# Kernel optimization log

Hardware: AMD Instinct MI355X
Metric: run time of the kernel (lower is better)

Reference implementation:

```python
import jax, jax.numpy as jnp
import numpy as np

H, DK, DV = 16, 64, 64

def setup_inputs() -> dict:
    key = jax.random.key(0)
    ks = jax.random.split(key, 5)
    S, E = 2048, 1024
    return {
        "x": jax.random.normal(ks[0], (S, E), jnp.float32),
        "Wq": jax.random.normal(ks[1], (H * DK, E), jnp.float32) * 0.02,
        "Wk": jax.random.normal(ks[2], (H * DK, E), jnp.float32) * 0.02,
        "Wv": jax.random.normal(ks[3], (H * DV, E), jnp.float32) * 0.02,
        "Wo": jax.random.normal(ks[4], (H * DV, H * DV), jnp.float32) * 0.02,
    }

def reference(x, Wq, Wk, Wv, Wo):
    S = x.shape[0]
    # Fused QKV projections (equivalent to per-head Linear with concatenated weights)
    Q = (x @ Wq.T).reshape(S, H, DK).transpose(1, 0, 2)  # [H,S,dk]
    K = (x @ Wk.T).reshape(S, H, DK).transpose(1, 0, 2)  # [H,S,dk]
    V = (x @ Wv.T).reshape(S, H, DV).transpose(1, 0, 2)  # [H,S,dv]
    scale = 1.0 / np.sqrt(DK).astype(np.float32)
    scores = jnp.einsum('hsd,htd->hst', Q, K) * scale    # [H,S,S]
    weights = jax.nn.softmax(scores, axis=-1)
    A = jnp.einsum('hst,htv->hsv', weights, V)           # [H,S,dv]
    A1 = A.transpose(1, 0, 2).reshape(S, H * DV)         # concat heads on last dim
    return A1 @ Wo.T
```

## Files before the change

### kernel.cpp

```cpp
#include <hip/hip_runtime.h>
#include <hip/hip_bf16.h>
#include <stdint.h>

typedef uint16_t u16;
typedef uint32_t u32;
typedef float    f32x4  __attribute__((ext_vector_type(4)));
typedef __bf16   bf16x8 __attribute__((ext_vector_type(8)));
typedef uint16_t u16x8  __attribute__((ext_vector_type(8)));
typedef uint16_t u16x4  __attribute__((ext_vector_type(4)));
typedef uint32_t u32x4  __attribute__((ext_vector_type(4)));

#define HH 16
#define SS 2048
#define EE 1024
#define DD 64

__device__ inline u16 f2bf(float f) {
  uint32_t u = __builtin_bit_cast(uint32_t, f);
  u += 0x7fff + ((u >> 16) & 1);
  return (u16)(u >> 16);
}
__device__ inline float bf2f(u16 b) {
  return __builtin_bit_cast(float, (uint32_t)b << 16);
}

__device__ inline u32 cvtpk(float lo, float hi) {
  u32 r;
  asm("v_cvt_pk_bf16_f32 %0, %1, %2" : "=v"(r) : "v"(lo), "v"(hi));
  return r;
}

__device__ inline void gload_lds16(const void* g, void* l) {
  __builtin_amdgcn_global_load_lds(
      (const __attribute__((address_space(1))) uint32_t*)g,
      (__attribute__((address_space(3))) uint32_t*)l, 16, 0, 0);
}

__global__ __launch_bounds__(256) void convert_kernel(
    const float* __restrict__ x,  const float* __restrict__ wq,
    const float* __restrict__ wk, const float* __restrict__ wv,
    const float* __restrict__ wo,
    u16* __restrict__ xb, u16* __restrict__ wqkvb, u16* __restrict__ wob) {
  const int64_t M1 = 1024 * 1024;
  int64_t e = ((int64_t)blockIdx.x * 256 + threadIdx.x) * 4;
  const float* src; u16* dst; int64_t off;
  if (e < 2 * M1)      { src = x;  dst = xb;           off = e; }
  else if (e < 3 * M1) { src = wq; dst = wqkvb;        off = e - 2 * M1; }
  else if (e < 4 * M1) { src = wk; dst = wqkvb + M1;   off = e - 3 * M1; }
  else if (e < 5 * M1) { src = wv; dst = wqkvb + 2*M1; off = e - 4 * M1; }
  else                 { src = wo; dst = wob;          off = e - 5 * M1; }
  float4 v = *(const float4*)(src + off);
  u16x4 o;
  o[0] = f2bf(v.x); o[1] = f2bf(v.y); o[2] = f2bf(v.z); o[3] = f2bf(v.w);
  *(u16x4*)(dst + off) = o;
}

template <int EPI, int K, int N, int BN>
__global__ __launch_bounds__(256, 4) void gemm_kernel(
    const u16* __restrict__ A, const u16* __restrict__ B,
    u16* __restrict__ q_ws, u16* __restrict__ k_ws, u16* __restrict__ vt_ws,
    float* __restrict__ Cout) {
  constexpr int BM = 64, BK = 64;
  constexpr int NFB = BN / 32;
  constexpr float C2 = 0.18033688f;
  __shared__ __align__(16) u16 As[BM * BK];
  __shared__ __align__(16) u16 Bs[BN * BK];
  const int t = threadIdx.x;
  const int lane = t & 63, w = t >> 6;
  const int wr = w >> 1, wc = w & 1;
  const int fr = lane & 15, fg = lane >> 4;

  const int nwg = gridDim.x * gridDim.y;
  const int bid = blockIdx.y * gridDim.x + blockIdx.x;
  const int swz = (bid & 7) * (nwg >> 3) + (bid >> 3);
  const int m0 = (swz / gridDim.x) * BM, n0 = (swz % gridDim.x) * BN;

  f32x4 acc[2][NFB] = {};

  for (int k0 = 0; k0 < K; k0 += BK) {
#pragma unroll
    for (int it = 0; it < 2; ++it) {
      const int c = t + it * 256, row = c >> 3, sch = (c & 7) ^ (row & 7);
      gload_lds16(A + (int64_t)(m0 + row) * K + k0 + sch * 8,
                  As + (c & ~63) * 8);
    }
#pragma unroll
    for (int it = 0; it < BN * 8 / 256; ++it) {
      const int c = t + it * 256, row = c >> 3, sch = (c & 7) ^ (row & 7);
      gload_lds16(B + (int64_t)(n0 + row) * K + k0 + sch * 8,
                  Bs + (c & ~63) * 8);
    }
    __syncthreads();
    bf16x8 af[2][2], bfr[NFB][2];
#pragma unroll
    for (int mi = 0; mi < 2; ++mi)
#pragma unroll
      for (int kc = 0; kc < 2; ++kc) {
        const int row = wr * 32 + mi * 16 + fr;
        const int cc = (kc * 4 + fg) ^ (row & 7);
        af[mi][kc] = __builtin_bit_cast(bf16x8, *(const u16x8*)&As[row * 64 + cc * 8]);
      }
#pragma unroll
    for (int ni = 0; ni < NFB; ++ni)
#pragma unroll
      for (int kc = 0; kc < 2; ++kc) {
        const int row = wc * (BN / 2) + ni * 16 + fr;
        const int cc = (kc * 4 + fg) ^ (row & 7);
        bfr[ni][kc] = __builtin_bit_cast(bf16x8, *(const u16x8*)&Bs[row * 64 + cc * 8]);
      }
#pragma unroll
    for (int kc = 0; kc < 2; ++kc)
#pragma unroll
      for (int mi = 0; mi < 2; ++mi)
#pragma unroll
        for (int ni = 0; ni < NFB; ++ni)
          acc[mi][ni] = __builtin_amdgcn_mfma_f32_16x16x32_bf16(
              af[mi][kc], bfr[ni][kc], acc[mi][ni], 0, 0, 0);
    __syncthreads();
  }

#pragma unroll
  for (int mi = 0; mi < 2; ++mi)
#pragma unroll
    for (int ni = 0; ni < NFB; ++ni)
#pragma unroll
      for (int r = 0; r < 4; ++r) {
        const int m = m0 + wr * 32 + mi * 16 + fg * 4 + r;
        const int n = n0 + wc * (BN / 2) + ni * 16 + fr;
        const float v = acc[mi][ni][r];
        if constexpr (EPI == 0) {
          const int which = n >> 10, nn = n & 1023, h = nn >> 6, d = nn & 63;
          if (which == 0)
            q_ws[((int64_t)h * SS + m) * DD + d] = f2bf(v * C2);
          else if (which == 1)
            k_ws[((int64_t)h * SS + m) * DD + d] = f2bf(v);
          else
            vt_ws[((int64_t)h * DD + d) * SS + m] = f2bf(v);
        } else {
          Cout[(int64_t)m * N + n] = v;
        }
      }
}

__global__ __launch_bounds__(256, 2) void attn_kernel(
    const u16* __restrict__ q_ws, const u16* __restrict__ k_ws,
    const u16* __restrict__ vt_ws, u16* __restrict__ opart,
    float* __restrict__ lsum) {
  constexpr int NTS = SS / 64 / 2;
  __shared__ __align__(16) u16 lds[16384];
  const int t = threadIdx.x;
  const int lane = t & 63, w = t >> 6;
  const int ql = lane & 15, g = lane >> 4;
  const int h = blockIdx.y, qb = blockIdx.x, sp = blockIdx.z;
  const int kt0 = sp * NTS;
  const int qbase = qb * 128 + w * 32;

  const u16* Qh = q_ws + ((int64_t)h * SS + qbase) * DD;
  const u16* Kh = k_ws + ((int64_t)h * SS + kt0 * 64) * DD;
  const u16* Vh = vt_ws + (int64_t)h * DD * SS + kt0 * 64;

  const int r0 = t >> 3, ch = t & 7, r1 = (t + 256) >> 3;
  const int sch0 = ch ^ (r0 & 7), sch1 = ch ^ (r1 & 7);
  const int64_t ko0 = (int64_t)r0 * DD + sch0 * 8;
  const int64_t ko1 = (int64_t)r1 * DD + sch1 * 8;
  const int64_t vo0 = (int64_t)r0 * SS + sch0 * 8;
  const int64_t vo1 = (int64_t)r1 * SS + sch1 * 8;
  const int dst0 = (t & ~63) * 8, dst1 = dst0 + 2048;

  bf16x8 qfl[2], qfh[2];
#pragma unroll
  for (int dd = 0; dd < 2; ++dd) {
    qfl[dd] = __builtin_bit_cast(
        bf16x8, *(const u16x8*)(Qh + ql * DD + dd * 32 + g * 8));
    qfh[dd] = __builtin_bit_cast(
        bf16x8, *(const u16x8*)(Qh + (ql + 16) * DD + dd * 32 + g * 8));
  }

  u16x8 ov;
#pragma unroll
  for (int j = 0; j < 8; ++j) ov[j] = 0x3F80;
  const bf16x8 onesf = __builtin_bit_cast(bf16x8, ov);

  f32x4 ol[4] = {}, oh[4] = {};
  f32x4 o_ll = {}, o_lh = {};

  auto qk = [&](f32x4 (&sl)[4], f32x4 (&sh)[4], const int kb_) {
    __builtin_amdgcn_s_setprio(1);
#pragma unroll
    for (int kb = 0; kb < 4; ++kb) {
      const int key = kb * 16 + ql;
      f32x4 zl = {}, zh = {};
#pragma unroll
      for (int dd = 0; dd < 2; ++dd) {
        bf16x8 kf = __builtin_bit_cast(
            bf16x8,
            *(const u16x8*)&lds[kb_ * 4096 + key * 64 +
                                (((dd * 4 + g) ^ (ql & 7)) * 8)]);
        zl = __builtin_amdgcn_mfma_f32_16x16x32_bf16(kf, qfl[dd], zl, 0, 0, 0);
        zh = __builtin_amdgcn_mfma_f32_16x16x32_bf16(kf, qfh[dd], zh, 0, 0, 0);
      }
      sl[kb] = zl; sh[kb] = zh;
    }
    __builtin_amdgcn_s_setprio(0);
  };

  auto smpv = [&](f32x4 (&sl)[4], f32x4 (&sh)[4], const int vb_) {
#pragma unroll
    for (int kb = 0; kb < 4; ++kb)
#pragma unroll
      for (int r = 0; r < 4; ++r) {
        sl[kb][r] = exp2f(sl[kb][r]);
        sh[kb][r] = exp2f(sh[kb][r]);
      }
#pragma unroll
    for (int ks = 0; ks < 2; ++ks) {
      u32 xl0 = cvtpk(sl[2 * ks][0], sl[2 * ks][1]);
      u32 xl1 = cvtpk(sl[2 * ks][2], sl[2 * ks][3]);
      u32 yl0 = cvtpk(sl[2 * ks + 1][0], sl[2 * ks + 1][1]);
      u32 yl1 = cvtpk(sl[2 * ks + 1][2], sl[2 * ks + 1][3]);
      asm("v_permlane32_swap_b32 %0, %1" : "+v"(xl0), "+v"(yl0));
      asm("v_permlane16_swap_b32 %0, %1" : "+v"(xl0), "+v"(yl0));
      asm("v_permlane32_swap_b32 %0, %1" : "+v"(xl1), "+v"(yl1));
      asm("v_permlane16_swap_b32 %0, %1" : "+v"(xl1), "+v"(yl1));
      u32x4 awl; awl[0] = xl0; awl[1] = xl1; awl[2] = yl0; awl[3] = yl1;
      const bf16x8 pal = __builtin_bit_cast(bf16x8, awl);
      u32 xh0 = cvtpk(sh[2 * ks][0], sh[2 * ks][1]);
      u32 xh1 = cvtpk(sh[2 * ks][2], sh[2 * ks][3]);
      u32 yh0 = cvtpk(sh[2 * ks + 1][0], sh[2 * ks + 1][1]);
      u32 yh1 = cvtpk(sh[2 * ks + 1][2], sh[2 * ks + 1][3]);
      asm("v_permlane32_swap_b32 %0, %1" : "+v"(xh0), "+v"(yh0));
      asm("v_permlane16_swap_b32 %0, %1" : "+v"(xh0), "+v"(yh0));
      asm("v_permlane32_swap_b32 %0, %1" : "+v"(xh1), "+v"(yh1));
      asm("v_permlane16_swap_b32 %0, %1" : "+v"(xh1), "+v"(yh1));
      u32x4 awh; awh[0] = xh0; awh[1] = xh1; awh[2] = yh0; awh[3] = yh1;
      const bf16x8 pah = __builtin_bit_cast(bf16x8, awh);
      __builtin_amdgcn_s_setprio(1);
      o_ll = __builtin_amdgcn_mfma_f32_16x16x32_bf16(pal, onesf, o_ll, 0, 0, 0);
      o_lh = __builtin_amdgcn_mfma_f32_16x16x32_bf16(pah, onesf, o_lh, 0, 0, 0);
#pragma unroll
      for (int nb = 0; nb < 4; ++nb) {
        const int dv = nb * 16 + ql;
        bf16x8 vf = __builtin_bit_cast(
            bf16x8,
            *(const u16x8*)&lds[8192 + vb_ * 4096 + dv * 64 +
                                (((ks * 4 + g) ^ (ql & 7)) * 8)]);
        ol[nb] = __builtin_amdgcn_mfma_f32_16x16x32_bf16(pal, vf, ol[nb], 0, 0, 0);
        oh[nb] = __builtin_amdgcn_mfma_f32_16x16x32_bf16(pah, vf, oh[nb], 0, 0, 0);
      }
      __builtin_amdgcn_s_setprio(0);
    }
  };

  gload_lds16(Kh + ko0, lds + dst0);
  gload_lds16(Kh + ko1, lds + dst1);

  f32x4 sAl[4], sAh[4], sBl[4], sBh[4];
#pragma unroll
  for (int tt = 0; tt < NTS; ++tt) {
    __syncthreads();
    if (tt + 1 < NTS) {
      const u16* Kn = Kh + (int64_t)(tt + 1) * 64 * DD;
      const int kb = ((tt + 1) & 1) * 4096;
      gload_lds16(Kn + ko0, lds + kb + dst0);
      gload_lds16(Kn + ko1, lds + kb + dst1);
    }
    {
      const u16* Vn = Vh + tt * 64;
      const int vb = 8192 + (tt & 1) * 4096;
      gload_lds16(Vn + vo0, lds + vb + dst0);
      gload_lds16(Vn + vo1, lds + vb + dst1);
    }
    if (tt & 1) {
      qk(sBl, sBh, tt & 1);
      smpv(sAl, sAh, (tt - 1) & 1);
    } else {
      qk(sAl, sAh, tt & 1);
      if (tt > 0) smpv(sBl, sBh, (tt - 1) & 1);
    }
  }
  __syncthreads();
  smpv(sBl, sBh, (NTS - 1) & 1);

  const int64_t rowbase = ((int64_t)sp * HH + h) * SS;
#pragma unroll
  for (int r = 0; r < 4; ++r) {
    const int q = qbase + g * 4 + r;
#pragma unroll
    for (int nb = 0; nb < 4; ++nb) {
      opart[(rowbase + q) * DD + nb * 16 + ql] = f2bf(ol[nb][r]);
      opart[(rowbase + q + 16) * DD + nb * 16 + ql] = f2bf(oh[nb][r]);
    }
  }
  if (ql == 0) {
#pragma unroll
    for (int r = 0; r < 4; ++r) {
      lsum[rowbase + qbase + g * 4 + r] = o_ll[r];
      lsum[rowbase + qbase + 16 + g * 4 + r] = o_lh[r];
    }
  }
}

__global__ __launch_bounds__(256) void combine_kernel(
    const u16* __restrict__ opart, const float* __restrict__ lsum,
    u16* __restrict__ a_ws) {
  const int rid = blockIdx.x * 4 + (threadIdx.x >> 6);
  const int lane = threadIdx.x & 63;
  const int h = rid >> 11, q = rid & 2047;
  const float inv = 1.0f / (lsum[rid] + lsum[HH * SS + rid]);
  const float o1 = bf2f(opart[(int64_t)rid * DD + lane]);
  const float o2 = bf2f(opart[((int64_t)HH * SS + rid) * DD + lane]);
  a_ws[(int64_t)q * (HH * DD) + h * DD + lane] = f2bf((o1 + o2) * inv);
}

extern "C" void kernel_launch(void* const* d_in, const int* in_sizes, int n_in,
                              void* d_out, int out_size, void* d_ws, size_t ws_size,
                              hipStream_t stream) {
  const float* x  = (const float*)d_in[0];
  const float* wq = (const float*)d_in[1];
  const float* wk = (const float*)d_in[2];
  const float* wv = (const float*)d_in[3];
  const float* wo = (const float*)d_in[4];
  char* ws = (char*)d_ws;
  const int64_t Mi = 1 << 20;
  u16* xb    = (u16*)(ws + 0 * Mi);
  u16* wqkv  = (u16*)(ws + 4 * Mi);
  u16* wob   = (u16*)(ws + 10 * Mi);
  u16* q_ws  = (u16*)(ws + 12 * Mi);
  u16* k_ws  = (u16*)(ws + 16 * Mi);
  u16* vt    = (u16*)(ws + 20 * Mi);
  u16*   opart = (u16*)(ws + 0 * Mi);
  float* lsv   = (float*)(ws + 8 * Mi);
  u16* a_ws  = (u16*)(ws + 12 * Mi);
  float* out = (float*)d_out;

  convert_kernel<<<6144, 256, 0, stream>>>(x, wq, wk, wv, wo, xb, wqkv, wob);

  gemm_kernel<0, 1024, 3072, 128><<<dim3(3072 / 128, 2048 / 64), 256, 0, stream>>>(
      xb, wqkv, q_ws, k_ws, vt, nullptr);

  attn_kernel<<<dim3(SS / 128, HH, 2), 256, 0, stream>>>(
      q_ws, k_ws, vt, opart, lsv);

  combine_kernel<<<HH * SS / 4, 256, 0, stream>>>(opart, lsv, a_ws);

  gemm_kernel<1, 1024, 1024, 64><<<dim3(1024 / 64, 2048 / 64), 256, 0, stream>>>(
      a_ws, wob, nullptr, nullptr, nullptr, out);
}
```

Measured before the change: 80.77 us.

## Drop LDS staging in attention, read K/V from global, split keys four ways

The attention kernel no longer double-buffers K and V tiles in shared memory with barriers. Each wave now reads its K and V fragments straight from global memory (through cache), and the key range is split into four chunks instead of two, which doubles the grid. Occupancy is raised to three blocks per SM, and the partial outputs for the extra splits are kept temporarily in the output buffer before combining. This removes LDS traffic and syncthreads overhead, but loses cross-wave reuse and swizzled conflict-free loads, so global and L2 traffic per block rises and combine reads twice as much data.

```diff
diff --git a/kernel.cpp b/kernel.cpp
--- a/kernel.cpp
+++ b/kernel.cpp
@@ -142,30 +142,20 @@
       }
 }
 
-__global__ __launch_bounds__(256, 2) void attn_kernel(
+__global__ __launch_bounds__(256, 3) void attn_kernel(
     const u16* __restrict__ q_ws, const u16* __restrict__ k_ws,
-    const u16* __restrict__ vt_ws, u16* __restrict__ opart,
-    float* __restrict__ lsum) {
-  constexpr int NTS = SS / 64 / 2;
-  __shared__ __align__(16) u16 lds[16384];
+    const u16* __restrict__ vt_ws, u16* __restrict__ op01,
+    u16* __restrict__ op23, float* __restrict__ lsum) {
+  constexpr int NTS = SS / 64 / 4;
   const int t = threadIdx.x;
   const int lane = t & 63, w = t >> 6;
   const int ql = lane & 15, g = lane >> 4;
   const int h = blockIdx.y, qb = blockIdx.x, sp = blockIdx.z;
-  const int kt0 = sp * NTS;
   const int qbase = qb * 128 + w * 32;
 
   const u16* Qh = q_ws + ((int64_t)h * SS + qbase) * DD;
-  const u16* Kh = k_ws + ((int64_t)h * SS + kt0 * 64) * DD;
-  const u16* Vh = vt_ws + (int64_t)h * DD * SS + kt0 * 64;
-
-  const int r0 = t >> 3, ch = t & 7, r1 = (t + 256) >> 3;
-  const int sch0 = ch ^ (r0 & 7), sch1 = ch ^ (r1 & 7);
-  const int64_t ko0 = (int64_t)r0 * DD + sch0 * 8;
-  const int64_t ko1 = (int64_t)r1 * DD + sch1 * 8;
-  const int64_t vo0 = (int64_t)r0 * SS + sch0 * 8;
-  const int64_t vo1 = (int64_t)r1 * SS + sch1 * 8;
-  const int dst0 = (t & ~63) * 8, dst1 = dst0 + 2048;
+  const u16* Kh = k_ws + ((int64_t)h * SS + sp * NTS * 64) * DD;
+  const u16* Vh = vt_ws + (int64_t)h * DD * SS + sp * NTS * 64;
 
   bf16x8 qfl[2], qfh[2];
 #pragma unroll
@@ -184,27 +174,27 @@
   f32x4 ol[4] = {}, oh[4] = {};
   f32x4 o_ll = {}, o_lh = {};
 
-  auto qk = [&](f32x4 (&sl)[4], f32x4 (&sh)[4], const int kb_) {
+  for (int tt = 0; tt < NTS; ++tt) {
+    const u16* Kt = Kh + (int64_t)tt * 64 * DD;
+    const u16* Vt = Vh + tt * 64;
+
+    f32x4 sl[4], sh[4];
     __builtin_amdgcn_s_setprio(1);
 #pragma unroll
     for (int kb = 0; kb < 4; ++kb) {
-      const int key = kb * 16 + ql;
       f32x4 zl = {}, zh = {};
 #pragma unroll
       for (int dd = 0; dd < 2; ++dd) {
         bf16x8 kf = __builtin_bit_cast(
             bf16x8,
-            *(const u16x8*)&lds[kb_ * 4096 + key * 64 +
-                                (((dd * 4 + g) ^ (ql & 7)) * 8)]);
+            *(const u16x8*)(Kt + (kb * 16 + ql) * DD + dd * 32 + g * 8));
         zl = __builtin_amdgcn_mfma_f32_16x16x32_bf16(kf, qfl[dd], zl, 0, 0, 0);
         zh = __builtin_amdgcn_mfma_f32_16x16x32_bf16(kf, qfh[dd], zh, 0, 0, 0);
       }
       sl[kb] = zl; sh[kb] = zh;
     }
     __builtin_amdgcn_s_setprio(0);
-  };
-
-  auto smpv = [&](f32x4 (&sl)[4], f32x4 (&sh)[4], const int vb_) {
+
 #pragma unroll
     for (int kb = 0; kb < 4; ++kb)
 #pragma unroll
@@ -212,6 +202,7 @@
         sl[kb][r] = exp2f(sl[kb][r]);
         sh[kb][r] = exp2f(sh[kb][r]);
       }
+
 #pragma unroll
     for (int ks = 0; ks < 2; ++ks) {
       u32 xl0 = cvtpk(sl[2 * ks][0], sl[2 * ks][1]);
@@ -242,74 +233,49 @@
         const int dv = nb * 16 + ql;
         bf16x8 vf = __builtin_bit_cast(
             bf16x8,
-            *(const u16x8*)&lds[8192 + vb_ * 4096 + dv * 64 +
-                                (((ks * 4 + g) ^ (ql & 7)) * 8)]);
+            *(const u16x8*)(Vt + (int64_t)dv * SS + (ks * 4 + g) * 8));
         ol[nb] = __builtin_amdgcn_mfma_f32_16x16x32_bf16(pal, vf, ol[nb], 0, 0, 0);
         oh[nb] = __builtin_amdgcn_mfma_f32_16x16x32_bf16(pah, vf, oh[nb], 0, 0, 0);
       }
       __builtin_amdgcn_s_setprio(0);
     }
-  };
-
-  gload_lds16(Kh + ko0, lds + dst0);
-  gload_lds16(Kh + ko1, lds + dst1);
-
-  f32x4 sAl[4], sAh[4], sBl[4], sBh[4];
-#pragma unroll
-  for (int tt = 0; tt < NTS; ++tt) {
-    __syncthreads();
-    if (tt + 1 < NTS) {
-      const u16* Kn = Kh + (int64_t)(tt + 1) * 64 * DD;
-      const int kb = ((tt + 1) & 1) * 4096;
-      gload_lds16(Kn + ko0, lds + kb + dst0);
-      gload_lds16(Kn + ko1, lds + kb + dst1);
-    }
-    {
-      const u16* Vn = Vh + tt * 64;
-      const int vb = 8192 + (tt & 1) * 4096;
-      gload_lds16(Vn + vo0, lds + vb + dst0);
-      gload_lds16(Vn + vo1, lds + vb + dst1);
-    }
-    if (tt & 1) {
-      qk(sBl, sBh, tt & 1);
-      smpv(sAl, sAh, (tt - 1) & 1);
-    } else {
-      qk(sAl, sAh, tt & 1);
-      if (tt > 0) smpv(sBl, sBh, (tt - 1) & 1);
-    }
-  }
-  __syncthreads();
-  smpv(sBl, sBh, (NTS - 1) & 1);
-
-  const int64_t rowbase = ((int64_t)sp * HH + h) * SS;
+  }
+
+  u16* ob = (sp & 2) ? op23 : op01;
+  const int64_t rowbase = ((int64_t)(sp & 1) * HH + h) * SS;
 #pragma unroll
   for (int r = 0; r < 4; ++r) {
     const int q = qbase + g * 4 + r;
 #pragma unroll
     for (int nb = 0; nb < 4; ++nb) {
-      opart[(rowbase + q) * DD + nb * 16 + ql] = f2bf(ol[nb][r]);
-      opart[(rowbase + q + 16) * DD + nb * 16 + ql] = f2bf(oh[nb][r]);
+      ob[(rowbase + q) * DD + nb * 16 + ql] = f2bf(ol[nb][r]);
+      ob[(rowbase + q + 16) * DD + nb * 16 + ql] = f2bf(oh[nb][r]);
     }
   }
   if (ql == 0) {
+    const int64_t lb = ((int64_t)sp * HH + h) * SS + qbase;
 #pragma unroll
     for (int r = 0; r < 4; ++r) {
-      lsum[rowbase + qbase + g * 4 + r] = o_ll[r];
-      lsum[rowbase + qbase + 16 + g * 4 + r] = o_lh[r];
+      lsum[lb + g * 4 + r] = o_ll[r];
+      lsum[lb + 16 + g * 4 + r] = o_lh[r];
     }
   }
 }
 
 __global__ __launch_bounds__(256) void combine_kernel(
-    const u16* __restrict__ opart, const float* __restrict__ lsum,
-    u16* __restrict__ a_ws) {
+    const u16* __restrict__ op01, const u16* __restrict__ op23,
+    const float* __restrict__ lsum, u16* __restrict__ a_ws) {
   const int rid = blockIdx.x * 4 + (threadIdx.x >> 6);
   const int lane = threadIdx.x & 63;
   const int h = rid >> 11, q = rid & 2047;
-  const float inv = 1.0f / (lsum[rid] + lsum[HH * SS + rid]);
-  const float o1 = bf2f(opart[(int64_t)rid * DD + lane]);
-  const float o2 = bf2f(opart[((int64_t)HH * SS + rid) * DD + lane]);
-  a_ws[(int64_t)q * (HH * DD) + h * DD + lane] = f2bf((o1 + o2) * inv);
+  const float inv = 1.0f / (lsum[rid] + lsum[HH * SS + rid] +
+                            lsum[2 * HH * SS + rid] + lsum[3 * HH * SS + rid]);
+  const float o0 = bf2f(op01[(int64_t)rid * DD + lane]);
+  const float o1 = bf2f(op01[((int64_t)HH * SS + rid) * DD + lane]);
+  const float o2 = bf2f(op23[(int64_t)rid * DD + lane]);
+  const float o3 = bf2f(op23[((int64_t)HH * SS + rid) * DD + lane]);
+  a_ws[(int64_t)q * (HH * DD) + h * DD + lane] =
+      f2bf((o0 + o1 + o2 + o3) * inv);
 }
 
 extern "C" void kernel_launch(void* const* d_in, const int* in_sizes, int n_in,
@@ -328,8 +294,9 @@
   u16* q_ws  = (u16*)(ws + 12 * Mi);
   u16* k_ws  = (u16*)(ws + 16 * Mi);
   u16* vt    = (u16*)(ws + 20 * Mi);
-  u16*   opart = (u16*)(ws + 0 * Mi);
-  float* lsv   = (float*)(ws + 8 * Mi);
+  u16*   op01 = (u16*)(ws + 0 * Mi);
+  u16*   op23 = (u16*)d_out;
+  float* lsv  = (float*)(ws + 8 * Mi);
   u16* a_ws  = (u16*)(ws + 12 * Mi);
   float* out = (float*)d_out;
 
@@ -338,10 +305,10 @@
   gemm_kernel<0, 1024, 3072, 128><<<dim3(3072 / 128, 2048 / 64), 256, 0, stream>>>(
       xb, wqkv, q_ws, k_ws, vt, nullptr);
 
-  attn_kernel<<<dim3(SS / 128, HH, 2), 256, 0, stream>>>(
-      q_ws, k_ws, vt, opart, lsv);
-
-  combine_kernel<<<HH * SS / 4, 256, 0, stream>>>(opart, lsv, a_ws);
+  attn_kernel<<<dim3(SS / 128, HH, 4), 256, 0, stream>>>(
+      q_ws, k_ws, vt, op01, op23, lsv);
+
+  combine_kernel<<<HH * SS / 4, 256, 0, stream>>>(op01, op23, lsv, a_ws);
 
   gemm_kernel<1, 1024, 1024, 64><<<dim3(1024 / 64, 2048 / 64), 256, 0, stream>>>(
       a_ws, wob, nullptr, nullptr, nullptr, out);
```

Result: slower. 114.3 us (+41.5%).
